# Optimization experiments

Hardware: AMD Instinct MI355X
Metric: run time of the kernel (lower is better)

The kernel has to match this reference:

```python
import jax, jax.numpy as jnp
import numpy as np
from jax import lax

EPS = 1e-5
F_CH = 32  # TIM future channels = int(256/8)
B_CH = 32  # TIM past channels (note: source bug -> these are zeroed, not shifted)


def inorm(x):
    # InstanceNorm3d (no affine): normalize each (b, c) over (T, H, W), biased var
    m = jnp.mean(x, axis=(2, 3, 4), keepdims=True)
    v = jnp.var(x, axis=(2, 3, 4), keepdims=True)
    return (x - m) * lax.rsqrt(v + EPS)


def conv1x1(x, w):
    # pointwise conv: x [B,C,T,H,W], w [O,C]
    return jnp.einsum('bcthw,oc->bothw', x, w)


def dwconv(x, w, pad):
    # depthwise 3D conv; w [C,1,kd,kh,kw], pad = [(pd,pd),(ph,ph),(pw,pw)]
    return lax.conv_general_dilated(
        x, w, window_strides=(1, 1, 1), padding=pad,
        feature_group_count=x.shape[1],
        dimension_numbers=('NCDHW', 'OIDHW', 'NCDHW'))


def tim(x):
    # Non-circular temporal interlacing. Faithful to source (past slice is a no-op):
    # channels [0:f]  <- x shifted from future (t+1), zero-padded at last frame
    # channels [f:f+b] <- zeros
    # channels [f+b:] <- identity
    f, b = F_CH, B_CH
    fut = jnp.concatenate([x[:, :f, 1:], jnp.zeros_like(x[:, :f, :1])], axis=2)
    mid = jnp.zeros_like(x[:, f:f + b])
    return jnp.concatenate([fut, mid, x[:, f + b:]], axis=1)


def setup_inputs() -> dict:
    key = jax.random.key(0)
    ks = jax.random.split(key, 7)
    cin, hid, cout = 64, 256, 64
    x = jax.random.normal(ks[0], (4, cin, 16, 64, 64), dtype=jnp.float32)
    w1 = jax.random.normal(ks[1], (hid, cin), dtype=jnp.float32) * 0.05
    w_dw_s = jax.random.normal(ks[2], (hid, 1, 1, 3, 3), dtype=jnp.float32) * 0.1
    w_dw_t = jax.random.normal(ks[3], (hid, 1, 3, 1, 1), dtype=jnp.float32) * 0.1
    w_se1 = jax.random.normal(ks[4], (hid // 4, hid), dtype=jnp.float32) * 0.05
    w_se2 = jax.random.normal(ks[5], (hid, hid // 4), dtype=jnp.float32) * 0.05
    w_proj = jax.random.normal(ks[6], (cout, hid), dtype=jnp.float32) * 0.05
    return {'x': x, 'w1': w1, 'w_dw_s': w_dw_s, 'w_dw_t': w_dw_t,
            'w_se1': w_se1, 'w_se2': w_se2, 'w_proj': w_proj}


def reference(x, w1, w_dw_s, w_dw_t, w_se1, w_se2, w_proj):
    shortcut = x
    # stage1: expand 1x1 conv + IN + ReLU
    h = jax.nn.relu(inorm(conv1x1(x, w1)))
    # temporal interlace (zero-FLOP channel shift)
    h = tim(h)
    # stage2: depthwise spatial (1,3,3) + IN + ReLU
    h = jax.nn.relu(inorm(dwconv(h, w_dw_s, [(0, 0), (1, 1), (1, 1)])))
    # stage3: depthwise temporal (3,1,1) + IN + ReLU
    h = jax.nn.relu(inorm(dwconv(h, w_dw_t, [(1, 1), (0, 0), (0, 0)])))
    # squeeze-excite
    y = jnp.mean(h, axis=(2, 3, 4), keepdims=True)           # [B,C,1,1,1]
    y = jax.nn.relu(jnp.einsum('bcthw,oc->bothw', y, w_se1))
    y = jax.nn.sigmoid(jnp.einsum('bcthw,oc->bothw', y, w_se2))
    h = h * y
    # proj 1x1 + IN, residual, maxpool (1,2,2)
    out = inorm(conv1x1(h, w_proj)) + shortcut
    out = lax.reduce_window(out, -jnp.inf, lax.max,
                            (1, 1, 1, 2, 2), (1, 1, 1, 2, 2), 'VALID')
    return out
```

## Files before the change

kernel.cpp:

```cpp
#include <hip/hip_runtime.h>
#include <hip/hip_bf16.h>

#define B_   4
#define CIN  64
#define HID  256
#define COUT 64
#define T_   16
#define H_   64
#define W_   64
#define HW_  (H_*W_)
#define THW  (T_*HW_)
#define EPS  1e-5f

typedef unsigned short ushort_t;
typedef unsigned int   uint_t;
typedef short bf16x8 __attribute__((ext_vector_type(8)));
typedef float f32x4  __attribute__((ext_vector_type(4)));

#define SA1   0
#define SB1   1024
#define SM3   4096
#define SIS3  5120
#define SSES  6144
#define SAL   7168
#define SBE   8192
__device__ float g_stats[10240];
__device__ float g_eps [4*1024*256];
__device__ float g_epss[4*1024*256];
__device__ ushort_t g_wpack[32768];

__device__ __forceinline__ float bf2f(ushort_t u) {
    return __uint_as_float(((uint_t)u) << 16);
}
__device__ __forceinline__ ushort_t f2bf(float f) {
    uint_t u = __float_as_uint(f);
    uint_t r = u + 0x7fffu + ((u >> 16) & 1u);
    return (ushort_t)(r >> 16);
}
__device__ __forceinline__ void unpacknorm2(uint2 k, float a, float bb, float* v) {
    uint_t uu[2] = {k.x, k.y};
    #pragma unroll
    for (int j = 0; j < 2; ++j) {
        v[2*j]   = fmaxf(fmaf(__uint_as_float(uu[j] << 16),         a, bb), 0.f);
        v[2*j+1] = fmaxf(fmaf(__uint_as_float(uu[j] & 0xffff0000u), a, bb), 0.f);
    }
}

__global__ __launch_bounds__(256) void k_prep(const float* __restrict__ w1,
                                              const float* __restrict__ wproj) {
    int idx = blockIdx.x*256 + threadIdx.x;
    {
        int j = idx & 7, lane = (idx>>3) & 63, ot = (idx>>9) & 3;
        int ks = (idx>>11) & 1, wv = idx >> 12;
        int ln = lane & 15, q = lane >> 4;
        int o = wv*64 + ot*16 + ln, k = ks*32 + q*8 + j;
        g_wpack[idx] = f2bf(w1[o*CIN + k]);
    }
    {
        int j = idx & 7, lane = (idx>>3) & 63, ot = (idx>>9) & 3, kg = idx >> 11;
        int ln = lane & 15, q = lane >> 4;
        int o = ot*16 + ln, k = kg*32 + q*8 + j;
        g_wpack[16384 + idx] = f2bf(wproj[o*HID + k]);
    }
}

__global__ __launch_bounds__(256) void k_expand(const float* __restrict__ x,
                                                ushort_t* __restrict__ h1, int b0) {
    union SMem {
        ushort_t Bs[64*72];
        float    red[2][256][16];
    };
    __shared__ SMem sm;
    const int tid = threadIdx.x;
    const int bb  = blockIdx.y, gb = b0 + bb;
    const int pos0 = blockIdx.x * 64;
    const int lane = tid & 63, wv = tid >> 6;
    const int q = lane >> 4, ln = lane & 15;

    bf16x8 af[2][4];
    #pragma unroll
    for (int ks = 0; ks < 2; ++ks)
        #pragma unroll
        for (int ot = 0; ot < 4; ++ot)
            af[ks][ot] = *(const bf16x8*)&g_wpack[(((wv*2+ks)*4+ot)<<9) + lane*8];

    #pragma unroll
    for (int i = 0; i < 4; ++i) {
        int lin = i*1024 + tid*4;
        int k = lin >> 6, n0 = lin & 63;
        float4 v = *(const float4*)&x[(size_t)(gb*CIN + k) * THW + pos0 + n0];
        ushort_t* d = &sm.Bs[k*72 + ((n0 + 16*((k>>3)&3)) & 63)];
        d[0] = f2bf(v.x); d[1] = f2bf(v.y); d[2] = f2bf(v.z); d[3] = f2bf(v.w);
    }
    __syncthreads();

    f32x4 acc[4][4];
    #pragma unroll
    for (int i = 0; i < 4; ++i)
        #pragma unroll
        for (int j = 0; j < 4; ++j)
            acc[i][j] = (f32x4){0.f,0.f,0.f,0.f};

    #pragma unroll
    for (int ks = 0; ks < 2; ++ks) {
        bf16x8 bfr[4];
        #pragma unroll
        for (int nt = 0; nt < 4; ++nt) {
            union { short s[8]; bf16x8 v; } bu;
            #pragma unroll
            for (int j = 0; j < 8; ++j) {
                int k = ks*32 + q*8 + j;
                int nn = (nt*16 + ln + 16*((k>>3)&3)) & 63;
                bu.s[j] = (short)sm.Bs[k*72 + nn];
            }
            bfr[nt] = bu.v;
        }
        #pragma unroll
        for (int ot = 0; ot < 4; ++ot)
            #pragma unroll
            for (int nt = 0; nt < 4; ++nt)
                acc[ot][nt] = __builtin_amdgcn_mfma_f32_16x16x32_bf16(
                    af[ks][ot], bfr[nt], acc[ot][nt], 0, 0, 0);
    }

    float sp_[16], ssp_[16];
    #pragma unroll
    for (int i = 0; i < 16; ++i) { sp_[i] = 0.f; ssp_[i] = 0.f; }

    #pragma unroll
    for (int ot = 0; ot < 4; ++ot)
        #pragma unroll
        for (int nt = 0; nt < 4; ++nt)
            #pragma unroll
            for (int r = 0; r < 4; ++r) {
                float vv = acc[ot][nt][r];
                int o = wv*64 + ot*16 + q*4 + r;
                int n = nt*16 + ln;
                h1[((size_t)bb*HID + o)*THW + pos0 + n] = f2bf(vv);
                sp_[ot*4+r] += vv;
                ssp_[ot*4+r] = fmaf(vv, vv, ssp_[ot*4+r]);
            }

    __syncthreads();
    #pragma unroll
    for (int i = 0; i < 16; ++i) {
        int o = wv*64 + (i>>2)*16 + q*4 + (i&3);
        sm.red[0][o][ln] = sp_[i];
        sm.red[1][o][ln] = ssp_[i];
    }
    __syncthreads();
    {
        float s = 0.f, ss = 0.f;
        #pragma unroll
        for (int l = 0; l < 16; ++l) {
            s  += sm.red[0][tid][l];
            ss += sm.red[1][tid][l];
        }
        size_t base = ((size_t)bb*1024 + blockIdx.x)*256 + tid;
        g_eps [base] = s;
        g_epss[base] = ss;
    }
}

__global__ __launch_bounds__(256) void k_red() {
    const int tid = threadIdx.x;
    const int cg  = blockIdx.x;
    const int bb  = blockIdx.y;
    const int ch  = cg*16 + (tid & 15);
    const int pb0 = tid >> 4;
    const float* ps  = &g_eps [((size_t)bb*1024)*256];
    const float* pss = &g_epss[((size_t)bb*1024)*256];
    float s = 0.f, ss = 0.f;
    #pragma unroll 8
    for (int it = 0; it < 64; ++it) {
        int pb = it*16 + pb0;
        s  += ps [(size_t)pb*256 + ch];
        ss += pss[(size_t)pb*256 + ch];
    }
    __shared__ float rs[256], rss[256];
    rs[tid] = s; rss[tid] = ss;
    __syncthreads();
    if (tid < 16) {
        float st = 0.f, sst = 0.f;
        #pragma unroll
        for (int k = 0; k < 16; ++k) { st += rs[tid + 16*k]; sst += rss[tid + 16*k]; }
        float m = st * (1.f/THW);
        float v = sst * (1.f/THW) - m*m;
        float is = 1.f / sqrtf(v + EPS);
        int bc = bb*HID + cg*16 + tid;
        g_stats[SA1 + bc] = is;
        g_stats[SB1 + bc] = -m * is;
    }
}

__global__ __launch_bounds__(1024) void k_mid(const ushort_t* __restrict__ h1,
                                              const float* __restrict__ wdws,
                                              const float* __restrict__ wdwt,
                                              ushort_t* __restrict__ h3) {
    const int tid = threadIdx.x;
    const int bc  = blockIdx.x;
    const int o   = bc & (HID-1);
    const int bb  = bc >> 8;
    const int wid = tid >> 6, lane = tid & 63;

    if (o >= 32 && o < 64) {
        if (tid == 0) {
            g_stats[SM3  + bc] = 0.f;
            g_stats[SIS3 + bc] = 1.f / sqrtf(EPS);
            g_stats[SSES + bc] = 0.f;
        }
        return;
    }

    __shared__ float pl[2][66*67];
    __shared__ float ls[16], lss[16];
    __shared__ float sa, sb;

    const float a1 = g_stats[SA1 + bc];
    const float b1 = g_stats[SB1 + bc];

    if (tid < 66) {
        #pragma unroll
        for (int b = 0; b < 2; ++b) {
            pl[b][tid]         = 0.f;
            pl[b][65*67 + tid] = 0.f;
            pl[b][tid*67]      = 0.f;
            pl[b][tid*67 + 65] = 0.f;
        }
    }

    const int fut = (o < 32) ? 1 : 0;
    const int y   = tid >> 4;
    const int x0  = (tid & 15) * 4;
    const ushort_t* chp = h1 + (size_t)bc * THW;
    const int lastp = fut ? (T_-2) : (T_-1);

    float wf[9];
    #pragma unroll
    for (int k = 0; k < 9; ++k) wf[k] = wdws[o*9 + k];

    uint2 sreg[2];
    sreg[0] = *(const uint2*)(chp + (size_t)fut*HW_ + tid*4);
    {
        float vv[4];
        unpacknorm2(sreg[0], a1, b1, vv);
        float* dst = &pl[0][(y+1)*67 + x0 + 1];
        #pragma unroll
        for (int i = 0; i < 4; ++i) dst[i] = vv[i];
    }
    sreg[1] = *(const uint2*)(chp + (size_t)(1+fut)*HW_ + tid*4);
    __syncthreads();

    uint2 keep[16];
    float s2 = 0.f, ss2 = 0.f;

    #pragma unroll
    for (int t = 0; t < T_; ++t) {
        if (t + 2 <= lastp)
            sreg[t & 1] = *(const uint2*)(chp + (size_t)(t+2+fut)*HW_ + tid*4);
        if (t + 1 <= lastp) {
            float vv[4];
            unpacknorm2(sreg[(t+1) & 1], a1, b1, vv);
            float* dst = &pl[(t+1) & 1][(y+1)*67 + x0 + 1];
            #pragma unroll
            for (int i = 0; i < 4; ++i) dst[i] = vv[i];
        }
        if (fut && t == T_-1) {
            keep[t] = (uint2){0u, 0u};
        } else {
            const float* plane = pl[t & 1];
            float v[3][6];
            #pragma unroll
            for (int dy = 0; dy < 3; ++dy) {
                const float* rp = &plane[(y + dy)*67 + x0];
                #pragma unroll
                for (int j = 0; j < 6; ++j) v[dy][j] = rp[j];
            }
            uint_t outp[2];
            #pragma unroll
            for (int i2 = 0; i2 < 2; ++i2) {
                float o0 = 0.f, o1 = 0.f;
                #pragma unroll
                for (int dy = 0; dy < 3; ++dy)
                    #pragma unroll
                    for (int dx = 0; dx < 3; ++dx) {
                        float w = wf[dy*3+dx];
                        o0 = fmaf(w, v[dy][2*i2 + dx],     o0);
                        o1 = fmaf(w, v[dy][2*i2 + 1 + dx], o1);
                    }
                ushort_t u0 = f2bf(o0), u1 = f2bf(o1);
                float r0 = bf2f(u0), r1 = bf2f(u1);
                s2 += r0 + r1; ss2 = fmaf(r0, r0, fmaf(r1, r1, ss2));
                outp[i2] = (uint_t)u0 | ((uint_t)u1 << 16);
            }
            keep[t].x = outp[0]; keep[t].y = outp[1];
        }
        __syncthreads();
    }

    {
        float s = s2, ss = ss2;
        #pragma unroll
        for (int m = 32; m > 0; m >>= 1) {
            s  += __shfl_xor(s,  m);
            ss += __shfl_xor(ss, m);
        }
        if (lane == 0) { ls[wid] = s; lss[wid] = ss; }
        __syncthreads();
        if (tid == 0) {
            float st = 0.f, sst = 0.f;
            #pragma unroll
            for (int i = 0; i < 16; ++i) { st += ls[i]; sst += lss[i]; }
            float m = st * (1.f/THW);
            float v = sst * (1.f/THW) - m*m;
            float is = 1.f / sqrtf(v + EPS);
            sa = is; sb = -m * is;
        }
        __syncthreads();
    }
    const float a2 = sa, b2 = sb;

    const float w0 = wdwt[o*3+0], w1 = wdwt[o*3+1], w2 = wdwt[o*3+2];
    ushort_t* op = h3 + (size_t)bc * THW + tid*4;

    float p[4], c[4], n[4];
    #pragma unroll
    for (int i = 0; i < 4; ++i) p[i] = 0.f;
    unpacknorm2(keep[0], a2, b2, c);
    unpacknorm2(keep[1], a2, b2, n);

    float s3 = 0.f, ss3 = 0.f;
    #pragma unroll
    for (int t = 0; t < T_; ++t) {
        uint_t outp[2];
        #pragma unroll
        for (int i2 = 0; i2 < 2; ++i2) {
            float o0 = fmaf(w0, p[2*i2],   fmaf(w1, c[2*i2],   w2 * n[2*i2]));
            float o1 = fmaf(w0, p[2*i2+1], fmaf(w1, c[2*i2+1], w2 * n[2*i2+1]));
            ushort_t u0 = f2bf(o0), u1 = f2bf(o1);
            float r0 = bf2f(u0), r1 = bf2f(u1);
            s3 += r0 + r1; ss3 = fmaf(r0, r0, fmaf(r1, r1, ss3));
            outp[i2] = (uint_t)u0 | ((uint_t)u1 << 16);
        }
        uint2 r; r.x = outp[0]; r.y = outp[1];
        *(uint2*)(op + (size_t)t*HW_) = r;

        #pragma unroll
        for (int i = 0; i < 4; ++i) { p[i] = c[i]; c[i] = n[i]; }
        if (t + 2 < T_) unpacknorm2(keep[t+2], a2, b2, n);
        else {
            #pragma unroll
            for (int i = 0; i < 4; ++i) n[i] = 0.f;
        }
        keep[t] = r;
    }

    {
        float s = s3, ss = ss3;
        #pragma unroll
        for (int m = 32; m > 0; m >>= 1) {
            s  += __shfl_xor(s,  m);
            ss += __shfl_xor(ss, m);
        }
        if (lane == 0) { ls[wid] = s; lss[wid] = ss; }
        __syncthreads();
        if (tid == 0) {
            float st = 0.f, sst = 0.f;
            #pragma unroll
            for (int i = 0; i < 16; ++i) { st += ls[i]; sst += lss[i]; }
            float m = st * (1.f/THW);
            float v = sst * (1.f/THW) - m*m;
            float is = 1.f / sqrtf(v + EPS);
            g_stats[SM3  + bc] = m;
            g_stats[SIS3 + bc] = is;
            sa = is; sb = -m * is;
        }
        __syncthreads();
    }

    const float a3 = sa, b3 = sb;
    float sse = 0.f;
    #pragma unroll
    for (int t = 0; t < T_; ++t) {
        uint_t uu[2] = {keep[t].x, keep[t].y};
        #pragma unroll
        for (int j = 0; j < 2; ++j) {
            sse += fmaxf(fmaf(__uint_as_float(uu[j] << 16),         a3, b3), 0.f);
            sse += fmaxf(fmaf(__uint_as_float(uu[j] & 0xffff0000u), a3, b3), 0.f);
        }
    }
    #pragma unroll
    for (int m = 32; m > 0; m >>= 1) sse += __shfl_xor(sse, m);
    if (lane == 0) ls[wid] = sse;
    __syncthreads();
    if (tid == 0) {
        float st = 0.f;
        #pragma unroll
        for (int i = 0; i < 16; ++i) st += ls[i];
        g_stats[SSES + bc] = st * (1.f/THW);
    }
}

__global__ __launch_bounds__(256) void k_semlp(const float* __restrict__ wse1,
                                               const float* __restrict__ wse2) {
    __shared__ float mv[HID];
    __shared__ float y1[64];
    const int bb = blockIdx.x, tid = threadIdx.x;
    mv[tid] = g_stats[SSES + bb*HID + tid];
    __syncthreads();
    if (tid < 64) {
        float acc = 0.f;
        #pragma unroll 8
        for (int c = 0; c < HID; ++c) acc = fmaf(wse1[tid*HID + c], mv[c], acc);
        y1[tid] = fmaxf(acc, 0.f);
    }
    __syncthreads();
    float z = 0.f;
    #pragma unroll
    for (int c = 0; c < 64; ++c) z = fmaf(wse2[tid*64 + c], y1[c], z);
    float se = 1.f / (1.f + expf(-z));
    const int bc = bb*HID + tid;
    float al = g_stats[SIS3 + bc] * se;
    if (tid >= 32 && tid < 64) al = 0.f;
    g_stats[SAL + bc] = al;
    g_stats[SBE + bc] = -g_stats[SM3 + bc] * al;
}

__global__ __launch_bounds__(256) void k_proj(const ushort_t* __restrict__ h3,
                                              float* __restrict__ proj) {
    __shared__ ushort_t Bs[64*136];
    const int tid = threadIdx.x;
    const int bb  = blockIdx.y;
    const int pos0 = blockIdx.x * 128;
    const int lane = tid & 63, wv = tid >> 6;
    const int q = lane >> 4, ln = lane & 15;

    f32x4 acc[4][2];
    #pragma unroll
    for (int i = 0; i < 4; ++i) {
        acc[i][0] = (f32x4){0.f,0.f,0.f,0.f};
        acc[i][1] = (f32x4){0.f,0.f,0.f,0.f};
    }

    for (int kc = 0; kc < 4; ++kc) {
        #pragma unroll
        for (int i = 0; i < 8; ++i) {
            int lin = i*1024 + tid*4;
            int kl = lin >> 7, n0 = lin & 127;
            int ch = bb*HID + kc*64 + kl;
            float al = g_stats[SAL + ch], be = g_stats[SBE + ch];
            ushort_t* d = &Bs[kl*136 + ((n0 + 16*((kl>>3)&7)) & 127)];
            if (al == 0.f) {
                d[0] = 0; d[1] = 0; d[2] = 0; d[3] = 0;
            } else {
                uint2 u = *(const uint2*)&h3[(size_t)ch * THW + pos0 + n0];
                float f0 = __uint_as_float(u.x << 16);
                float f1 = __uint_as_float(u.x & 0xffff0000u);
                float f2 = __uint_as_float(u.y << 16);
                float f3 = __uint_as_float(u.y & 0xffff0000u);
                d[0] = f2bf(fmaxf(fmaf(f0, al, be), 0.f));
                d[1] = f2bf(fmaxf(fmaf(f1, al, be), 0.f));
                d[2] = f2bf(fmaxf(fmaf(f2, al, be), 0.f));
                d[3] = f2bf(fmaxf(fmaf(f3, al, be), 0.f));
            }
        }
        __syncthreads();

        #pragma unroll
        for (int ks = 0; ks < 2; ++ks) {
            int kg = kc*2 + ks;
            bf16x8 af[4];
            #pragma unroll
            for (int ot = 0; ot < 4; ++ot)
                af[ot] = *(const bf16x8*)&g_wpack[16384 + ((kg*4+ot)<<9) + lane*8];
            bf16x8 bfr[2];
            #pragma unroll
            for (int nt = 0; nt < 2; ++nt) {
                union { short s[8]; bf16x8 v; } bu;
                #pragma unroll
                for (int j = 0; j < 8; ++j) {
                    int kl = ks*32 + q*8 + j;
                    int nn = (wv*32 + nt*16 + ln + 16*((kl>>3)&7)) & 127;
                    bu.s[j] = (short)Bs[kl*136 + nn];
                }
                bfr[nt] = bu.v;
            }
            #pragma unroll
            for (int ot = 0; ot < 4; ++ot)
                #pragma unroll
                for (int nt = 0; nt < 2; ++nt)
                    acc[ot][nt] = __builtin_amdgcn_mfma_f32_16x16x32_bf16(
                        af[ot], bfr[nt], acc[ot][nt], 0, 0, 0);
        }
        __syncthreads();
    }

    #pragma unroll
    for (int ot = 0; ot < 4; ++ot)
        #pragma unroll
        for (int nt = 0; nt < 2; ++nt)
            #pragma unroll
            for (int r = 0; r < 4; ++r) {
                int o = ot*16 + q*4 + r;
                int n = wv*32 + nt*16 + ln;
                proj[((size_t)bb*COUT + o)*THW + pos0 + n] = acc[ot][nt][r];
            }
}

__global__ __launch_bounds__(1024) void k_final(const float* __restrict__ proj,
                                                const float* __restrict__ x,
                                                float* __restrict__ out, int b0) {
    const int bo  = blockIdx.x;
    const int tid = threadIdx.x;
    const float* p = proj + (size_t)bo * THW;

    float s = 0.f, ss = 0.f;
    #pragma unroll
    for (int i = 0; i < THW/(1024*4); ++i) {
        float4 u = *(const float4*)(p + i*4096 + tid*4);
        s += u.x; ss = fmaf(u.x, u.x, ss);
        s += u.y; ss = fmaf(u.y, u.y, ss);
        s += u.z; ss = fmaf(u.z, u.z, ss);
        s += u.w; ss = fmaf(u.w, u.w, ss);
    }
    #pragma unroll
    for (int off = 32; off > 0; off >>= 1) {
        s  += __shfl_down(s,  off, 64);
        ss += __shfl_down(ss, off, 64);
    }
    __shared__ float ls[16], lss[16];
    __shared__ float sa, sb;
    int wid = tid >> 6, lane = tid & 63;
    if (lane == 0) { ls[wid] = s; lss[wid] = ss; }
    __syncthreads();
    if (tid == 0) {
        float st = 0.f, sst = 0.f;
        #pragma unroll
        for (int i = 0; i < 16; ++i) { st += ls[i]; sst += lss[i]; }
        float m = st * (1.f/THW);
        float v = sst * (1.f/THW) - m*m;
        float is = 1.f / sqrtf(v + EPS);
        sa = is; sb = -m * is;
    }
    __syncthreads();
    const float a = sa, bb = sb;

    const size_t gbase = (size_t)(b0*COUT + bo) * THW;
    float* op = out + (size_t)(b0*COUT + bo) * (T_*1024);
    #pragma unroll
    for (int i = 0; i < 16; ++i) {
        int idx = i*1024 + tid;
        int xx = idx & 31, yy = (idx >> 5) & 31, t = idx >> 10;
        float m = -3.4e38f;
        #pragma unroll
        for (int r = 0; r < 2; ++r) {
            size_t off = (size_t)t*HW_ + (size_t)(2*yy + r)*W_ + 2*xx;
            float2 p2 = *(const float2*)(p + off);
            float2 x2 = *(const float2*)(x + gbase + off);
            float v0 = fmaf(p2.x, a, bb) + x2.x;
            float v1 = fmaf(p2.y, a, bb) + x2.y;
            m = fmaxf(m, fmaxf(v0, v1));
        }
        op[idx] = m;
    }
}

extern "C" void kernel_launch(void* const* d_in, const int* in_sizes, int n_in,
                              void* d_out, int out_size, void* d_ws, size_t ws_size,
                              hipStream_t stream) {
    const float* x     = (const float*)d_in[0];
    const float* w1    = (const float*)d_in[1];
    const float* wdws  = (const float*)d_in[2];
    const float* wdwt  = (const float*)d_in[3];
    const float* wse1  = (const float*)d_in[4];
    const float* wse2  = (const float*)d_in[5];
    const float* wproj = (const float*)d_in[6];
    float* out = (float*)d_out;

    const size_t perb = 2ull * HID * THW * sizeof(ushort_t);
    int nb = (ws_size >= 4*perb) ? 4 : (ws_size >= 2*perb) ? 2 : 1;

    k_prep<<<64, 256, 0, stream>>>(w1, wproj);

    for (int b0 = 0; b0 < B_; b0 += nb) {
        char* ws = (char*)d_ws;
        ushort_t* h1   = (ushort_t*)ws;
        ushort_t* h3   = h1;
        float*    proj = (float*)(ws + (size_t)nb * HID*THW*2);

        k_expand<<<dim3(THW/64, nb), 256, 0, stream>>>(x, h1, b0);
        k_red   <<<dim3(16, nb), 256, 0, stream>>>();
        k_mid   <<<nb*HID, 1024, 0, stream>>>(h1, wdws, wdwt, h3);
        k_semlp <<<nb, 256, 0, stream>>>(wse1, wse2);
        k_proj  <<<dim3(THW/128, nb), 256, 0, stream>>>(h3, proj);
        k_final <<<nb*COUT, 1024, 0, stream>>>(proj, x, out, b0);
    }
}
```

Baseline: 354.9 us.

## Quad-buffer depthwise planes, process two frames per barrier, skip zeroed channel blocks

The spatial depthwise stage now keeps four shared-memory plane buffers and handles two time frames per iteration, which halves the number of block-wide barriers and prefetches further ahead. The grid no longer launches blocks for the always-zero middle channels. Their constant statistics are written by the reduction kernel instead. This doubles the shared memory per block to about 70 KB, which may limit residency, and it adds more register pressure from the extra prefetch registers.

Result: no change. 351.2 us (-1.0%).

```diff
diff --git a/kernel.cpp b/kernel.cpp
--- a/kernel.cpp
+++ b/kernel.cpp
@@ -187,9 +187,15 @@
         float m = st * (1.f/THW);
         float v = sst * (1.f/THW) - m*m;
         float is = 1.f / sqrtf(v + EPS);
-        int bc = bb*HID + cg*16 + tid;
+        int ch_ = cg*16 + tid;
+        int bc = bb*HID + ch_;
         g_stats[SA1 + bc] = is;
         g_stats[SB1 + bc] = -m * is;
+        if (ch_ >= 32 && ch_ < 64) {
+            g_stats[SM3  + bc] = 0.f;
+            g_stats[SIS3 + bc] = 1.f / sqrtf(EPS);
+            g_stats[SSES + bc] = 0.f;
+        }
     }
 }
 
@@ -198,21 +204,13 @@
                                               const float* __restrict__ wdwt,
                                               ushort_t* __restrict__ h3) {
     const int tid = threadIdx.x;
-    const int bc  = blockIdx.x;
-    const int o   = bc & (HID-1);
-    const int bb  = bc >> 8;
+    const int oc  = blockIdx.x;
+    const int o   = (oc < 32) ? oc : oc + 32;
+    const int bb  = blockIdx.y;
+    const int bc  = bb*HID + o;
     const int wid = tid >> 6, lane = tid & 63;
 
-    if (o >= 32 && o < 64) {
-        if (tid == 0) {
-            g_stats[SM3  + bc] = 0.f;
-            g_stats[SIS3 + bc] = 1.f / sqrtf(EPS);
-            g_stats[SSES + bc] = 0.f;
-        }
-        return;
-    }
-
-    __shared__ float pl[2][66*67];
+    __shared__ float pl[4][66*67];
     __shared__ float ls[16], lss[16];
     __shared__ float sa, sb;
 
@@ -221,7 +219,7 @@
 
     if (tid < 66) {
         #pragma unroll
-        for (int b = 0; b < 2; ++b) {
+        for (int b = 0; b < 4; ++b) {
             pl[b][tid]         = 0.f;
             pl[b][65*67 + tid] = 0.f;
             pl[b][tid*67]      = 0.f;
@@ -239,63 +237,79 @@
     #pragma unroll
     for (int k = 0; k < 9; ++k) wf[k] = wdws[o*9 + k];
 
-    uint2 sreg[2];
-    sreg[0] = *(const uint2*)(chp + (size_t)fut*HW_ + tid*4);
-    {
+    uint2 sreg[4];
+    sreg[0] = *(const uint2*)(chp + (size_t)(0+fut)*HW_ + tid*4);
+    sreg[1] = *(const uint2*)(chp + (size_t)(1+fut)*HW_ + tid*4);
+    #pragma unroll
+    for (int p = 0; p < 2; ++p) {
         float vv[4];
-        unpacknorm2(sreg[0], a1, b1, vv);
-        float* dst = &pl[0][(y+1)*67 + x0 + 1];
+        unpacknorm2(sreg[p], a1, b1, vv);
+        float* dst = &pl[p][(y+1)*67 + x0 + 1];
         #pragma unroll
         for (int i = 0; i < 4; ++i) dst[i] = vv[i];
     }
-    sreg[1] = *(const uint2*)(chp + (size_t)(1+fut)*HW_ + tid*4);
+    sreg[2] = *(const uint2*)(chp + (size_t)(2+fut)*HW_ + tid*4);
+    sreg[3] = *(const uint2*)(chp + (size_t)(3+fut)*HW_ + tid*4);
     __syncthreads();
 
     uint2 keep[16];
     float s2 = 0.f, ss2 = 0.f;
 
     #pragma unroll
-    for (int t = 0; t < T_; ++t) {
-        if (t + 2 <= lastp)
-            sreg[t & 1] = *(const uint2*)(chp + (size_t)(t+2+fut)*HW_ + tid*4);
-        if (t + 1 <= lastp) {
-            float vv[4];
-            unpacknorm2(sreg[(t+1) & 1], a1, b1, vv);
-            float* dst = &pl[(t+1) & 1][(y+1)*67 + x0 + 1];
-            #pragma unroll
-            for (int i = 0; i < 4; ++i) dst[i] = vv[i];
-        }
-        if (fut && t == T_-1) {
-            keep[t] = (uint2){0u, 0u};
-        } else {
-            const float* plane = pl[t & 1];
-            float v[3][6];
-            #pragma unroll
-            for (int dy = 0; dy < 3; ++dy) {
-                const float* rp = &plane[(y + dy)*67 + x0];
+    for (int it = 0; it < 8; ++it) {
+        {
+            int pA = 2*it + 4, pB = 2*it + 5;
+            if (pA <= lastp)
+                sreg[pA & 3] = *(const uint2*)(chp + (size_t)(pA+fut)*HW_ + tid*4);
+            if (pB <= lastp)
+                sreg[pB & 3] = *(const uint2*)(chp + (size_t)(pB+fut)*HW_ + tid*4);
+        }
+        #pragma unroll
+        for (int w = 0; w < 2; ++w) {
+            int wp = 2*it + 2 + w;
+            if (wp <= lastp) {
+                float vv[4];
+                unpacknorm2(sreg[wp & 3], a1, b1, vv);
+                float* dst = &pl[wp & 3][(y+1)*67 + x0 + 1];
                 #pragma unroll
-                for (int j = 0; j < 6; ++j) v[dy][j] = rp[j];
+                for (int i = 0; i < 4; ++i) dst[i] = vv[i];
             }
-            uint_t outp[2];
-            #pragma unroll
-            for (int i2 = 0; i2 < 2; ++i2) {
-                float o0 = 0.f, o1 = 0.f;
+        }
+        #pragma unroll
+        for (int cpi = 0; cpi < 2; ++cpi) {
+            int t = 2*it + cpi;
+            if (fut && t == T_-1) {
+                keep[t] = (uint2){0u, 0u};
+            } else {
+                const float* plane = pl[t & 3];
+                float v[3][6];
                 #pragma unroll
-                for (int dy = 0; dy < 3; ++dy)
+                for (int dy = 0; dy < 3; ++dy) {
+                    const float* rp = &plane[(y + dy)*67 + x0];
                     #pragma unroll
-                    for (int dx = 0; dx < 3; ++dx) {
-                        float w = wf[dy*3+dx];
-                        o0 = fmaf(w, v[dy][2*i2 + dx],     o0);
-                        o1 = fmaf(w, v[dy][2*i2 + 1 + dx], o1);
-                    }
-                ushort_t u0 = f2bf(o0), u1 = f2bf(o1);
-                float r0 = bf2f(u0), r1 = bf2f(u1);
-                s2 += r0 + r1; ss2 = fmaf(r0, r0, fmaf(r1, r1, ss2));
-                outp[i2] = (uint_t)u0 | ((uint_t)u1 << 16);
+                    for (int j = 0; j < 6; ++j) v[dy][j] = rp[j];
+                }
+                uint_t outp[2];
+                #pragma unroll
+                for (int i2 = 0; i2 < 2; ++i2) {
+                    float o0 = 0.f, o1 = 0.f;
+                    #pragma unroll
+                    for (int dy = 0; dy < 3; ++dy)
+                        #pragma unroll
+                        for (int dx = 0; dx < 3; ++dx) {
+                            float w = wf[dy*3+dx];
+                            o0 = fmaf(w, v[dy][2*i2 + dx],     o0);
+                            o1 = fmaf(w, v[dy][2*i2 + 1 + dx], o1);
+                        }
+                    ushort_t u0 = f2bf(o0), u1 = f2bf(o1);
+                    float r0 = bf2f(u0), r1 = bf2f(u1);
+                    s2 += r0 + r1; ss2 = fmaf(r0, r0, fmaf(r1, r1, ss2));
+                    outp[i2] = (uint_t)u0 | ((uint_t)u1 << 16);
+                }
+                keep[t].x = outp[0]; keep[t].y = outp[1];
             }
-            keep[t].x = outp[0]; keep[t].y = outp[1];
-        }
-        __syncthreads();
+        }
+        if (it < 7) __syncthreads();
     }
 
     {
@@ -590,7 +604,7 @@
 
         k_expand<<<dim3(THW/64, nb), 256, 0, stream>>>(x, h1, b0);
         k_red   <<<dim3(16, nb), 256, 0, stream>>>();
-        k_mid   <<<nb*HID, 1024, 0, stream>>>(h1, wdws, wdwt, h3);
+        k_mid   <<<dim3(224, nb), 1024, 0, stream>>>(h1, wdws, wdwt, h3);
         k_semlp <<<nb, 256, 0, stream>>>(wse1, wse2);
         k_proj  <<<dim3(THW/128, nb), 256, 0, stream>>>(h3, proj);
         k_final <<<nb*COUT, 1024, 0, stream>>>(proj, x, out, b0);
```
